# Kernel optimization log

Measured on AMD Instinct MI355X. Metric: run time of the kernel, lower is better.

Reference implementation:

```python
import jax, jax.numpy as jnp
import numpy as np

INPUT_SIZE = 40960
HIDDEN = 256
BATCH = 32768
ACTIVE = 32  # active features per position (~one per piece)


def setup_inputs() -> dict:
    key = jax.random.key(0)
    ks = jax.random.split(key, 11)
    return {
        "white_idx": jax.random.randint(ks[0], (BATCH, ACTIVE), 0, INPUT_SIZE, dtype=jnp.int32),
        "black_idx": jax.random.randint(ks[1], (BATCH, ACTIVE), 0, INPUT_SIZE, dtype=jnp.int32),
        "stm": jax.random.randint(ks[2], (BATCH, 1), 0, 2).astype(jnp.float32),
        "ft_w": jax.random.normal(ks[3], (INPUT_SIZE, HIDDEN), dtype=jnp.float32) * 0.02,
        "ft_b": jax.random.normal(ks[4], (HIDDEN,), dtype=jnp.float32) * 0.02,
        "l1_w": jax.random.normal(ks[5], (32, 2 * HIDDEN), dtype=jnp.float32) * 0.05,
        "l1_b": jax.random.normal(ks[6], (32,), dtype=jnp.float32) * 0.05,
        "l2_w": jax.random.normal(ks[7], (32, 32), dtype=jnp.float32) * 0.05,
        "l2_b": jax.random.normal(ks[8], (32,), dtype=jnp.float32) * 0.05,
        "l3_w": jax.random.normal(ks[9], (1, 32), dtype=jnp.float32) * 0.05,
        "l3_b": jax.random.normal(ks[10], (1,), dtype=jnp.float32) * 0.05,
    }


def _ft(idx, ft_w, ft_b):
    # sparse-COO (unit values) @ ft.weight^T + bias == gather rows of the
    # [input_size, hidden] table and sum over active features.
    return ft_w[idx].sum(axis=1) + ft_b  # [B, H]


def reference(white_idx, black_idx, stm, ft_w, ft_b, l1_w, l1_b, l2_w, l2_b, l3_w, l3_b):
    w = jnp.clip(_ft(white_idx, ft_w, ft_b), 0.0, 1.0)
    b = jnp.clip(_ft(black_idx, ft_w, ft_b), 0.0, 1.0)
    acc = stm * jnp.concatenate([w, b], axis=1) + (1.0 - stm) * jnp.concatenate([b, w], axis=1)
    x = jnp.clip(acc @ l1_w.T + l1_b, 0.0, 1.0)
    x = jnp.clip(x @ l2_w.T + l2_b, 0.0, 1.0)
    return x @ l3_w.T + l3_b  # [B, 1]
```

## Files before the change

kernel.cpp:

```cpp
#include <hip/hip_runtime.h>

#define BATCH 32768
#define HID 256
#define ACT 32
#define NROWS 40960

#define TBL_BYTES ((size_t)NROWS * HID * 2)
#define ACT_BYTES ((size_t)BATCH * 512 * 4)

__global__ __launch_bounds__(256) void nnue_cvt_kernel(
    const float* __restrict__ ft_w, unsigned short* __restrict__ tbl)
{
    const int g  = blockIdx.y;
    const int tx = blockIdx.x * 256 + threadIdx.x;
    const int row = tx >> 2;
    const int c8  = tx & 3;
    const float* __restrict__ src = ft_w + (size_t)row * HID + g * 32 + c8 * 8;
    unsigned int o[8];
    #pragma unroll
    for (int j = 0; j < 8; ++j) {
        unsigned int u = __float_as_uint(src[j]);
        u = u + 0x7FFFu + ((u >> 16) & 1u);
        o[j] = u >> 16;
    }
    uint4 pack;
    pack.x = o[0] | (o[1] << 16);
    pack.y = o[2] | (o[3] << 16);
    pack.z = o[4] | (o[5] << 16);
    pack.w = o[6] | (o[7] << 16);
    *(uint4*)(tbl + ((size_t)g * NROWS + row) * 32 + c8 * 8) = pack;
}

__global__ __launch_bounds__(256, 4) void nnue_ft_kernel(
    const int* __restrict__ widx, const int* __restrict__ bidx,
    const float* __restrict__ stm,
    const unsigned short* __restrict__ tbl, const float* __restrict__ ft_b,
    float* __restrict__ act)
{
    const int bid = blockIdx.x;
    const int g   = bid & 7;
    const int pt  = bid >> 3;
    const int t   = threadIdx.x;
    const int w   = t >> 6;
    const int q   = t & 63;
    const int r   = q >> 3;
    const int c   = q & 7;

    __shared__ int   sidx[16][64];
    __shared__ float sstm[16];

    #pragma unroll
    for (int k = 0; k < 2; ++k) {
        const int u = t + k * 256;
        const int p = u >> 5, rr = u & 31;
        sidx[p][rr]      = widx[(size_t)(pt * 16 + p) * ACT + rr];
        sidx[p][32 + rr] = bidx[(size_t)(pt * 16 + p) * ACT + rr];
    }
    if (t < 16) sstm[t] = stm[pt * 16 + t];
    __syncthreads();

    const unsigned short* __restrict__ tg = tbl + (size_t)g * NROWS * 32;
    const float4 bv = ((const float4*)ft_b)[g * 8 + c];

    for (int i = 0; i < 4; ++i) {
        const int p   = w * 4 + i;
        const int pos = pt * 16 + p;

        uint2 raw[8];
        #pragma unroll
        for (int k = 0; k < 8; ++k) {
            const int rowid = sidx[p][k * 8 + r];
            raw[k] = *(const uint2*)(tg + ((size_t)rowid << 5) + (c << 2));
        }

        float a0=0.f,a1=0.f,a2=0.f,a3=0.f;
        float b0=0.f,b1=0.f,b2=0.f,b3=0.f;
        #pragma unroll
        for (int k = 0; k < 4; ++k) {
            a0 += __uint_as_float(raw[k].x << 16);
            a1 += __uint_as_float(raw[k].x & 0xFFFF0000u);
            a2 += __uint_as_float(raw[k].y << 16);
            a3 += __uint_as_float(raw[k].y & 0xFFFF0000u);
        }
        #pragma unroll
        for (int k = 4; k < 8; ++k) {
            b0 += __uint_as_float(raw[k].x << 16);
            b1 += __uint_as_float(raw[k].x & 0xFFFF0000u);
            b2 += __uint_as_float(raw[k].y << 16);
            b3 += __uint_as_float(raw[k].y & 0xFFFF0000u);
        }

        #pragma unroll
        for (int m = 8; m < 64; m <<= 1) {
            a0 += __shfl_xor(a0, m, 64);
            a1 += __shfl_xor(a1, m, 64);
            a2 += __shfl_xor(a2, m, 64);
            a3 += __shfl_xor(a3, m, 64);
            b0 += __shfl_xor(b0, m, 64);
            b1 += __shfl_xor(b1, m, 64);
            b2 += __shfl_xor(b2, m, 64);
            b3 += __shfl_xor(b3, m, 64);
        }

        const float w0 = fminf(fmaxf(a0 + bv.x, 0.f), 1.f);
        const float w1 = fminf(fmaxf(a1 + bv.y, 0.f), 1.f);
        const float w2 = fminf(fmaxf(a2 + bv.z, 0.f), 1.f);
        const float w3 = fminf(fmaxf(a3 + bv.w, 0.f), 1.f);
        const float z0 = fminf(fmaxf(b0 + bv.x, 0.f), 1.f);
        const float z1 = fminf(fmaxf(b1 + bv.y, 0.f), 1.f);
        const float z2 = fminf(fmaxf(b2 + bv.z, 0.f), 1.f);
        const float z3 = fminf(fmaxf(b3 + bv.w, 0.f), 1.f);

        if (r == 0) {
            const bool s = (sstm[p] != 0.0f);
            float* dst = act + (size_t)pos * 512 + g * 32 + (c << 2);
            float4 wa; wa.x=w0; wa.y=w1; wa.z=w2; wa.w=w3;
            float4 za; za.x=z0; za.y=z1; za.z=z2; za.w=z3;
            *(float4*)(dst + (s ? 0 : 256)) = wa;
            *(float4*)(dst + (s ? 256 : 0)) = za;
        }
    }
}

__global__ __launch_bounds__(256, 4) void nnue_mlp_kernel(
    const float* __restrict__ act,
    const float* __restrict__ l1_w, const float* __restrict__ l1_b,
    const float* __restrict__ l2_w, const float* __restrict__ l2_b,
    const float* __restrict__ l3_w, const float* __restrict__ l3_b,
    float* __restrict__ out)
{
    const int bb = blockIdx.x;
    const int t  = threadIdx.x;

    __shared__ float4 sact[8 * 128];
    __shared__ float  x1s[8][32];
    __shared__ float  x2s[8][32];

    const float4* __restrict__ ga = (const float4*)(act + (size_t)bb * 8 * 512);
    #pragma unroll
    for (int k = 0; k < 4; ++k) sact[t + k * 256] = ga[t + k * 256];
    __syncthreads();

    {
        const int o  = t >> 3;
        const int l8 = t & 7;
        const float4* __restrict__ wrow = (const float4*)(l1_w + o * 512);
        float pacc[8] = {0.f,0.f,0.f,0.f,0.f,0.f,0.f,0.f};
        #pragma unroll
        for (int j = 0; j < 16; ++j) {
            const int i4 = l8 + j * 8;
            const float4 wv = wrow[i4];
            #pragma unroll
            for (int p = 0; p < 8; ++p) {
                const float4 a = sact[p * 128 + i4];
                pacc[p] += wv.x*a.x + wv.y*a.y + wv.z*a.z + wv.w*a.w;
            }
        }
        #pragma unroll
        for (int p = 0; p < 8; ++p) {
            pacc[p] += __shfl_down(pacc[p], 4, 8);
            pacc[p] += __shfl_down(pacc[p], 2, 8);
            pacc[p] += __shfl_down(pacc[p], 1, 8);
        }
        if (l8 == 0) {
            const float bo = l1_b[o];
            #pragma unroll
            for (int p = 0; p < 8; ++p)
                x1s[p][o] = fminf(fmaxf(pacc[p] + bo, 0.f), 1.f);
        }
    }
    __syncthreads();

    {
        const int p  = t >> 5;
        const int oo = t & 31;
        const float* __restrict__ wr = l2_w + oo * 32;
        float s2 = l2_b[oo];
        #pragma unroll
        for (int j = 0; j < 32; ++j) s2 += x1s[p][j] * wr[j];
        x2s[p][oo] = fminf(fmaxf(s2, 0.f), 1.f);
    }
    __syncthreads();

    if (t < 8) {
        float s3 = l3_b[0];
        #pragma unroll
        for (int j = 0; j < 32; ++j) s3 += x2s[t][j] * l3_w[j];
        out[bb * 8 + t] = s3;
    }
}

__device__ __forceinline__ float4 clip4(float4 v) {
    v.x = fminf(fmaxf(v.x, 0.0f), 1.0f);
    v.y = fminf(fmaxf(v.y, 0.0f), 1.0f);
    v.z = fminf(fmaxf(v.z, 0.0f), 1.0f);
    v.w = fminf(fmaxf(v.w, 0.0f), 1.0f);
    return v;
}
__device__ __forceinline__ void acc4(float4& a, const float4 v) {
    a.x += v.x; a.y += v.y; a.z += v.z; a.w += v.w;
}

__global__ __launch_bounds__(256, 4) void nnue_fwd_fallback(
    const int* __restrict__ widx, const int* __restrict__ bidx,
    const float* __restrict__ stm,
    const float* __restrict__ ft_w, const float* __restrict__ ft_b,
    const float* __restrict__ l1_w, const float* __restrict__ l1_b,
    const float* __restrict__ l2_w, const float* __restrict__ l2_b,
    const float* __restrict__ l3_w, const float* __restrict__ l3_b,
    float* __restrict__ out)
{
    const int bb = blockIdx.x;
    const int t  = threadIdx.x;
    const int w  = t >> 6;
    const int q  = t & 63;

    __shared__ float4 accbuf[4][128];
    __shared__ float  x1s[4][32];
    __shared__ float  x2s[4][32];

    const int pos = bb * 4 + w;
    int myidx;
    if (q < 32) myidx = widx[pos * ACT + q];
    else        myidx = bidx[pos * ACT + (q - 32)];

    const float4* __restrict__ ftw4 = (const float4*)ft_w;
    const float4  bias = ((const float4*)ft_b)[q];
    float4 accW = bias, accB = bias;

    #pragma unroll
    for (int r0 = 0; r0 < 32; r0 += 8) {
        float4 vw[8], vb[8];
        #pragma unroll
        for (int i = 0; i < 8; ++i) {
            const int rw = __builtin_amdgcn_readlane(myidx, r0 + i);
            vw[i] = ftw4[(size_t)rw * 64 + q];
        }
        #pragma unroll
        for (int i = 0; i < 8; ++i) {
            const int rb = __builtin_amdgcn_readlane(myidx, 32 + r0 + i);
            vb[i] = ftw4[(size_t)rb * 64 + q];
        }
        #pragma unroll
        for (int i = 0; i < 8; ++i) { acc4(accW, vw[i]); acc4(accB, vb[i]); }
    }

    const bool s = (stm[pos] != 0.0f);
    accbuf[w][(s ? 0 : 64) + q] = clip4(accW);
    accbuf[w][(s ? 64 : 0) + q] = clip4(accB);
    __syncthreads();

    {
        const int o  = t >> 3;
        const int l8 = t & 7;
        const float4* __restrict__ wrow = (const float4*)(l1_w + o * 512);
        float p0 = 0.f, p1 = 0.f, p2 = 0.f, p3 = 0.f;
        #pragma unroll
        for (int j = 0; j < 16; ++j) {
            const int i4 = l8 + j * 8;
            const float4 wv = wrow[i4];
            const float4 a0 = accbuf[0][i4];
            const float4 a1 = accbuf[1][i4];
            const float4 a2 = accbuf[2][i4];
            const float4 a3 = accbuf[3][i4];
            p0 += wv.x*a0.x + wv.y*a0.y + wv.z*a0.z + wv.w*a0.w;
            p1 += wv.x*a1.x + wv.y*a1.y + wv.z*a1.z + wv.w*a1.w;
            p2 += wv.x*a2.x + wv.y*a2.y + wv.z*a2.z + wv.w*a2.w;
            p3 += wv.x*a3.x + wv.y*a3.y + wv.z*a3.z + wv.w*a3.w;
        }
        p0 += __shfl_down(p0, 4, 8); p0 += __shfl_down(p0, 2, 8); p0 += __shfl_down(p0, 1, 8);
        p1 += __shfl_down(p1, 4, 8); p1 += __shfl_down(p1, 2, 8); p1 += __shfl_down(p1, 1, 8);
        p2 += __shfl_down(p2, 4, 8); p2 += __shfl_down(p2, 2, 8); p2 += __shfl_down(p2, 1, 8);
        p3 += __shfl_down(p3, 4, 8); p3 += __shfl_down(p3, 2, 8); p3 += __shfl_down(p3, 1, 8);
        if (l8 == 0) {
            const float bo = l1_b[o];
            x1s[0][o] = fminf(fmaxf(p0 + bo, 0.0f), 1.0f);
            x1s[1][o] = fminf(fmaxf(p1 + bo, 0.0f), 1.0f);
            x1s[2][o] = fminf(fmaxf(p2 + bo, 0.0f), 1.0f);
            x1s[3][o] = fminf(fmaxf(p3 + bo, 0.0f), 1.0f);
        }
    }
    __syncthreads();

    if (t < 128) {
        const int g  = t >> 5;
        const int oo = t & 31;
        const float* __restrict__ wr = l2_w + oo * 32;
        float p = l2_b[oo];
        #pragma unroll
        for (int j = 0; j < 32; ++j) p += x1s[g][j] * wr[j];
        x2s[g][oo] = fminf(fmaxf(p, 0.0f), 1.0f);
    }
    __syncthreads();

    if (t < 4) {
        float p = l3_b[0];
        #pragma unroll
        for (int j = 0; j < 32; ++j) p += x2s[t][j] * l3_w[j];
        out[bb * 4 + t] = p;
    }
}

extern "C" void kernel_launch(void* const* d_in, const int* in_sizes, int n_in,
                              void* d_out, int out_size, void* d_ws, size_t ws_size,
                              hipStream_t stream) {
    const int*   widx = (const int*)d_in[0];
    const int*   bidx = (const int*)d_in[1];
    const float* stm  = (const float*)d_in[2];
    const float* ft_w = (const float*)d_in[3];
    const float* ft_b = (const float*)d_in[4];
    const float* l1_w = (const float*)d_in[5];
    const float* l1_b = (const float*)d_in[6];
    const float* l2_w = (const float*)d_in[7];
    const float* l2_b = (const float*)d_in[8];
    const float* l3_w = (const float*)d_in[9];
    const float* l3_b = (const float*)d_in[10];
    float* out = (float*)d_out;

    if (ws_size >= TBL_BYTES + ACT_BYTES) {
        unsigned short* tbl = (unsigned short*)d_ws;
        float* act = (float*)((char*)d_ws + TBL_BYTES);
        nnue_cvt_kernel<<<dim3(640, 8), 256, 0, stream>>>(ft_w, tbl);
        nnue_ft_kernel<<<(BATCH / 16) * 8, 256, 0, stream>>>(widx, bidx, stm, tbl, ft_b, act);
        nnue_mlp_kernel<<<BATCH / 8, 256, 0, stream>>>(act, l1_w, l1_b, l2_w, l2_b, l3_w, l3_b, out);
    } else {
        nnue_fwd_fallback<<<BATCH / 4, 256, 0, stream>>>(
            widx, bidx, stm, ft_w, ft_b, l1_w, l1_b, l2_w, l2_b, l3_w, l3_b, out);
    }
}
```

Before: 136.6 us.

## Give each ft lane a whole position and double MLP positions per block

The feature-transform kernel now maps each group of 8 lanes to one position, so every lane gathers all 32 white and 32 black rows itself. This removes the cross-lane shuffle reduction and the r==0 store predicate. Row offsets are prescaled into shared memory and read as int4, and occupancy launch bounds go up to 8 blocks per CU. The MLP kernel handles 16 positions per block instead of 8 to reuse each l1 weight load more, at the cost of more registers and LDS per block.

```diff
diff --git a/kernel.cpp b/kernel.cpp
--- a/kernel.cpp
+++ b/kernel.cpp
@@ -31,7 +31,9 @@
     *(uint4*)(tbl + ((size_t)g * NROWS + row) * 32 + c8 * 8) = pack;
 }
 
-__global__ __launch_bounds__(256, 4) void nnue_ft_kernel(
+#define LDU2(o) (*(const uint2*)(tg + (unsigned int)(o) + cb))
+
+__global__ __launch_bounds__(256, 8) void nnue_ft_kernel(
     const int* __restrict__ widx, const int* __restrict__ bidx,
     const float* __restrict__ stm,
     const unsigned short* __restrict__ tbl, const float* __restrict__ ft_b,
@@ -41,85 +43,77 @@
     const int g   = bid & 7;
     const int pt  = bid >> 3;
     const int t   = threadIdx.x;
-    const int w   = t >> 6;
     const int q   = t & 63;
-    const int r   = q >> 3;
+    const int p   = (t >> 6) * 8 + (q >> 3);
     const int c   = q & 7;
 
-    __shared__ int   sidx[16][64];
-    __shared__ float sstm[16];
-
-    #pragma unroll
-    for (int k = 0; k < 2; ++k) {
-        const int u = t + k * 256;
-        const int p = u >> 5, rr = u & 31;
-        sidx[p][rr]      = widx[(size_t)(pt * 16 + p) * ACT + rr];
-        sidx[p][32 + rr] = bidx[(size_t)(pt * 16 + p) * ACT + rr];
-    }
-    if (t < 16) sstm[t] = stm[pt * 16 + t];
-    __syncthreads();
-
-    const unsigned short* __restrict__ tg = tbl + (size_t)g * NROWS * 32;
+    __shared__ int   soff[32][68];
+    __shared__ float sstm[32];
+
+    #pragma unroll
+    for (int k = 0; k < 4; ++k) {
+        const int u  = t + k * 256;
+        const int pp = u >> 5, rr = u & 31;
+        soff[pp][rr]      = widx[(size_t)(pt * 32 + pp) * ACT + rr] << 6;
+        soff[pp][32 + rr] = bidx[(size_t)(pt * 32 + pp) * ACT + rr] << 6;
+    }
+    if (t < 32) sstm[t] = stm[pt * 32 + t];
+    __syncthreads();
+
+    const char* __restrict__ tg = (const char*)(tbl + (size_t)g * NROWS * 32);
+    const unsigned int cb = (unsigned int)(c << 3);
+    const int4* __restrict__ sview = (const int4*)(&soff[p][0]);
+
+    float a0=0.f,a1=0.f,a2=0.f,a3=0.f;
+    float b0=0.f,b1=0.f,b2=0.f,b3=0.f;
+
+    #pragma unroll
+    for (int blk = 0; blk < 4; ++blk) {
+        const int4 oA = sview[blk * 2];
+        const int4 oB = sview[blk * 2 + 1];
+        uint2 v[8];
+        v[0] = LDU2(oA.x); v[1] = LDU2(oA.y); v[2] = LDU2(oA.z); v[3] = LDU2(oA.w);
+        v[4] = LDU2(oB.x); v[5] = LDU2(oB.y); v[6] = LDU2(oB.z); v[7] = LDU2(oB.w);
+        #pragma unroll
+        for (int i = 0; i < 8; ++i) {
+            a0 += __uint_as_float(v[i].x << 16);
+            a1 += __uint_as_float(v[i].x & 0xFFFF0000u);
+            a2 += __uint_as_float(v[i].y << 16);
+            a3 += __uint_as_float(v[i].y & 0xFFFF0000u);
+        }
+    }
+    #pragma unroll
+    for (int blk = 4; blk < 8; ++blk) {
+        const int4 oA = sview[blk * 2];
+        const int4 oB = sview[blk * 2 + 1];
+        uint2 v[8];
+        v[0] = LDU2(oA.x); v[1] = LDU2(oA.y); v[2] = LDU2(oA.z); v[3] = LDU2(oA.w);
+        v[4] = LDU2(oB.x); v[5] = LDU2(oB.y); v[6] = LDU2(oB.z); v[7] = LDU2(oB.w);
+        #pragma unroll
+        for (int i = 0; i < 8; ++i) {
+            b0 += __uint_as_float(v[i].x << 16);
+            b1 += __uint_as_float(v[i].x & 0xFFFF0000u);
+            b2 += __uint_as_float(v[i].y << 16);
+            b3 += __uint_as_float(v[i].y & 0xFFFF0000u);
+        }
+    }
+
     const float4 bv = ((const float4*)ft_b)[g * 8 + c];
-
-    for (int i = 0; i < 4; ++i) {
-        const int p   = w * 4 + i;
-        const int pos = pt * 16 + p;
-
-        uint2 raw[8];
-        #pragma unroll
-        for (int k = 0; k < 8; ++k) {
-            const int rowid = sidx[p][k * 8 + r];
-            raw[k] = *(const uint2*)(tg + ((size_t)rowid << 5) + (c << 2));
-        }
-
-        float a0=0.f,a1=0.f,a2=0.f,a3=0.f;
-        float b0=0.f,b1=0.f,b2=0.f,b3=0.f;
-        #pragma unroll
-        for (int k = 0; k < 4; ++k) {
-            a0 += __uint_as_float(raw[k].x << 16);
-            a1 += __uint_as_float(raw[k].x & 0xFFFF0000u);
-            a2 += __uint_as_float(raw[k].y << 16);
-            a3 += __uint_as_float(raw[k].y & 0xFFFF0000u);
-        }
-        #pragma unroll
-        for (int k = 4; k < 8; ++k) {
-            b0 += __uint_as_float(raw[k].x << 16);
-            b1 += __uint_as_float(raw[k].x & 0xFFFF0000u);
-            b2 += __uint_as_float(raw[k].y << 16);
-            b3 += __uint_as_float(raw[k].y & 0xFFFF0000u);
-        }
-
-        #pragma unroll
-        for (int m = 8; m < 64; m <<= 1) {
-            a0 += __shfl_xor(a0, m, 64);
-            a1 += __shfl_xor(a1, m, 64);
-            a2 += __shfl_xor(a2, m, 64);
-            a3 += __shfl_xor(a3, m, 64);
-            b0 += __shfl_xor(b0, m, 64);
-            b1 += __shfl_xor(b1, m, 64);
-            b2 += __shfl_xor(b2, m, 64);
-            b3 += __shfl_xor(b3, m, 64);
-        }
-
-        const float w0 = fminf(fmaxf(a0 + bv.x, 0.f), 1.f);
-        const float w1 = fminf(fmaxf(a1 + bv.y, 0.f), 1.f);
-        const float w2 = fminf(fmaxf(a2 + bv.z, 0.f), 1.f);
-        const float w3 = fminf(fmaxf(a3 + bv.w, 0.f), 1.f);
-        const float z0 = fminf(fmaxf(b0 + bv.x, 0.f), 1.f);
-        const float z1 = fminf(fmaxf(b1 + bv.y, 0.f), 1.f);
-        const float z2 = fminf(fmaxf(b2 + bv.z, 0.f), 1.f);
-        const float z3 = fminf(fmaxf(b3 + bv.w, 0.f), 1.f);
-
-        if (r == 0) {
-            const bool s = (sstm[p] != 0.0f);
-            float* dst = act + (size_t)pos * 512 + g * 32 + (c << 2);
-            float4 wa; wa.x=w0; wa.y=w1; wa.z=w2; wa.w=w3;
-            float4 za; za.x=z0; za.y=z1; za.z=z2; za.w=z3;
-            *(float4*)(dst + (s ? 0 : 256)) = wa;
-            *(float4*)(dst + (s ? 256 : 0)) = za;
-        }
-    }
+    float4 wa, za;
+    wa.x = fminf(fmaxf(a0 + bv.x, 0.f), 1.f);
+    wa.y = fminf(fmaxf(a1 + bv.y, 0.f), 1.f);
+    wa.z = fminf(fmaxf(a2 + bv.z, 0.f), 1.f);
+    wa.w = fminf(fmaxf(a3 + bv.w, 0.f), 1.f);
+    za.x = fminf(fmaxf(b0 + bv.x, 0.f), 1.f);
+    za.y = fminf(fmaxf(b1 + bv.y, 0.f), 1.f);
+    za.z = fminf(fmaxf(b2 + bv.z, 0.f), 1.f);
+    za.w = fminf(fmaxf(b3 + bv.w, 0.f), 1.f);
+
+    const int  pos = pt * 32 + p;
+    const bool s   = (sstm[p] != 0.0f);
+    float* dst = act + (size_t)pos * 512 + g * 32 + (c << 2);
+    *(float4*)(dst + (s ? 0 : 256)) = wa;
+    *(float4*)(dst + (s ? 256 : 0)) = za;
 }
 
 __global__ __launch_bounds__(256, 4) void nnue_mlp_kernel(
@@ -132,32 +126,34 @@
     const int bb = blockIdx.x;
     const int t  = threadIdx.x;
 
-    __shared__ float4 sact[8 * 128];
-    __shared__ float  x1s[8][32];
-    __shared__ float  x2s[8][32];
-
-    const float4* __restrict__ ga = (const float4*)(act + (size_t)bb * 8 * 512);
-    #pragma unroll
-    for (int k = 0; k < 4; ++k) sact[t + k * 256] = ga[t + k * 256];
+    __shared__ float4 sact[16 * 128];
+    __shared__ float  x1s[16][33];
+    __shared__ float  x2s[16][33];
+
+    const float4* __restrict__ ga = (const float4*)(act + (size_t)bb * 16 * 512);
+    #pragma unroll
+    for (int k = 0; k < 8; ++k) sact[t + k * 256] = ga[t + k * 256];
     __syncthreads();
 
     {
         const int o  = t >> 3;
         const int l8 = t & 7;
         const float4* __restrict__ wrow = (const float4*)(l1_w + o * 512);
-        float pacc[8] = {0.f,0.f,0.f,0.f,0.f,0.f,0.f,0.f};
+        float pacc[16];
+        #pragma unroll
+        for (int p = 0; p < 16; ++p) pacc[p] = 0.f;
         #pragma unroll
         for (int j = 0; j < 16; ++j) {
             const int i4 = l8 + j * 8;
             const float4 wv = wrow[i4];
             #pragma unroll
-            for (int p = 0; p < 8; ++p) {
+            for (int p = 0; p < 16; ++p) {
                 const float4 a = sact[p * 128 + i4];
                 pacc[p] += wv.x*a.x + wv.y*a.y + wv.z*a.z + wv.w*a.w;
             }
         }
         #pragma unroll
-        for (int p = 0; p < 8; ++p) {
+        for (int p = 0; p < 16; ++p) {
             pacc[p] += __shfl_down(pacc[p], 4, 8);
             pacc[p] += __shfl_down(pacc[p], 2, 8);
             pacc[p] += __shfl_down(pacc[p], 1, 8);
@@ -165,14 +161,15 @@
         if (l8 == 0) {
             const float bo = l1_b[o];
             #pragma unroll
-            for (int p = 0; p < 8; ++p)
+            for (int p = 0; p < 16; ++p)
                 x1s[p][o] = fminf(fmaxf(pacc[p] + bo, 0.f), 1.f);
         }
     }
     __syncthreads();
 
-    {
-        const int p  = t >> 5;
+    #pragma unroll
+    for (int h = 0; h < 2; ++h) {
+        const int p  = h * 8 + (t >> 5);
         const int oo = t & 31;
         const float* __restrict__ wr = l2_w + oo * 32;
         float s2 = l2_b[oo];
@@ -182,11 +179,11 @@
     }
     __syncthreads();
 
-    if (t < 8) {
+    if (t < 16) {
         float s3 = l3_b[0];
         #pragma unroll
         for (int j = 0; j < 32; ++j) s3 += x2s[t][j] * l3_w[j];
-        out[bb * 8 + t] = s3;
+        out[bb * 16 + t] = s3;
     }
 }
 
@@ -321,8 +318,8 @@
         unsigned short* tbl = (unsigned short*)d_ws;
         float* act = (float*)((char*)d_ws + TBL_BYTES);
         nnue_cvt_kernel<<<dim3(640, 8), 256, 0, stream>>>(ft_w, tbl);
-        nnue_ft_kernel<<<(BATCH / 16) * 8, 256, 0, stream>>>(widx, bidx, stm, tbl, ft_b, act);
-        nnue_mlp_kernel<<<BATCH / 8, 256, 0, stream>>>(act, l1_w, l1_b, l2_w, l2_b, l3_w, l3_b, out);
+        nnue_ft_kernel<<<(BATCH / 32) * 8, 256, 0, stream>>>(widx, bidx, stm, tbl, ft_b, act);
+        nnue_mlp_kernel<<<BATCH / 16, 256, 0, stream>>>(act, l1_w, l1_b, l2_w, l2_b, l3_w, l3_b, out);
     } else {
         nnue_fwd_fallback<<<BATCH / 4, 256, 0, stream>>>(
             widx, bidx, stm, ft_w, ft_b, l1_w, l1_b, l2_w, l2_b, l3_w, l3_b, out);
```

After: 151.4 us. 10.9% more time.
